# Kernel optimization log

Hardware: AMD Instinct MI355X
Metric: run time of the kernel (lower is better)

Reference implementation:

```python
import jax, jax.numpy as jnp
import numpy as np

N_PROP = 2048
N_CLS = 81  # background + 80 foreground classes
IMG_W, IMG_H = 1333.0, 800.0
SCORE_THRESH = 0.05
NMS_THRESH = 0.5
DET_PER_IMG = 100
BBOX_CLIP = float(np.log(1000.0 / 16.0))
TO_REMOVE = 1.0


def setup_inputs() -> dict:
    key = jax.random.key(0)
    k1, k2, k3, k4, k5, k6 = jax.random.split(key, 6)
    class_logits = jax.random.normal(k1, (N_PROP, N_CLS), jnp.float32)
    box_regression = jax.random.normal(k2, (N_PROP, N_CLS * 4), jnp.float32)
    # valid xyxy proposals inside the image
    x1 = jax.random.uniform(k3, (N_PROP,), jnp.float32, 0.0, IMG_W * 0.7)
    y1 = jax.random.uniform(k4, (N_PROP,), jnp.float32, 0.0, IMG_H * 0.7)
    w = jax.random.uniform(k5, (N_PROP,), jnp.float32, 16.0, IMG_W * 0.3)
    h = jax.random.uniform(k6, (N_PROP,), jnp.float32, 16.0, IMG_H * 0.3)
    proposals = jnp.stack([x1, y1, x1 + w, y1 + h], axis=-1)
    return {"class_logits": class_logits, "box_regression": box_regression, "proposals": proposals}


def decode_boxes(reg, props):
    # BoxCoder.decode with weights (10,10,5,5); reg: [N, C*4] -> [N, C, 4]
    widths = props[:, 2] - props[:, 0] + TO_REMOVE
    heights = props[:, 3] - props[:, 1] + TO_REMOVE
    ctr_x = props[:, 0] + 0.5 * widths
    ctr_y = props[:, 1] + 0.5 * heights
    r = reg.reshape(reg.shape[0], -1, 4)
    dx = r[..., 0] / 10.0
    dy = r[..., 1] / 10.0
    dw = jnp.minimum(r[..., 2] / 5.0, BBOX_CLIP)
    dh = jnp.minimum(r[..., 3] / 5.0, BBOX_CLIP)
    pcx = dx * widths[:, None] + ctr_x[:, None]
    pcy = dy * heights[:, None] + ctr_y[:, None]
    pw = jnp.exp(dw) * widths[:, None]
    ph = jnp.exp(dh) * heights[:, None]
    return jnp.stack([pcx - 0.5 * pw, pcy - 0.5 * ph,
                      pcx + 0.5 * pw - TO_REMOVE, pcy + 0.5 * ph - TO_REMOVE], axis=-1)


def pairwise_iou(b):
    # b: [N,4] xyxy -> [N,N] IoU with +1 pixel convention
    area = (b[:, 2] - b[:, 0] + TO_REMOVE) * (b[:, 3] - b[:, 1] + TO_REMOVE)
    lt = jnp.maximum(b[:, None, :2], b[None, :, :2])
    rb = jnp.minimum(b[:, None, 2:], b[None, :, 2:])
    wh = jnp.clip(rb - lt + TO_REMOVE, 0.0)
    inter = wh[..., 0] * wh[..., 1]
    return inter / (area[:, None] + area[None, :] - inter)


def nms_keep(boxes, scores, valid, thresh):
    # returns boolean keep mask (fixed shape) equivalent to greedy NMS on valid boxes
    n = scores.shape[0]
    order = jnp.argsort(-scores)
    b = boxes[order]
    v = valid[order]
    iou = pairwise_iou(b)  # [N,N]
    idx = jnp.arange(n)

    def step(suppressed, inp):
        row, vi, i = inp
        keep_i = vi & jnp.logical_not(suppressed[i])
        suppressed = suppressed | (keep_i & (row > thresh) & (idx > i))
        return suppressed, keep_i

    _, keep_sorted = jax.lax.scan(step, jnp.zeros(n, bool), (iou, v, idx))
    return jnp.zeros(n, bool).at[order].set(keep_sorted)


def _forward(class_logits, box_regression, proposals):
    probs = jax.nn.softmax(class_logits, axis=-1)          # [N, C]
    boxes = decode_boxes(box_regression, proposals)        # [N, C, 4]
    # clip_to_image (remove_empty=False)
    boxes = jnp.stack([jnp.clip(boxes[..., 0], 0.0, IMG_W - TO_REMOVE),
                       jnp.clip(boxes[..., 1], 0.0, IMG_H - TO_REMOVE),
                       jnp.clip(boxes[..., 2], 0.0, IMG_W - TO_REMOVE),
                       jnp.clip(boxes[..., 3], 0.0, IMG_H - TO_REMOVE)], axis=-1)
    # drop background class 0; class-major layout [C-1, N, ...]
    boxes_c = jnp.transpose(boxes[:, 1:, :], (1, 0, 2))    # [C-1, N, 4]
    scores_c = probs[:, 1:].T                              # [C-1, N]
    valid = scores_c > SCORE_THRESH
    keep = jax.vmap(nms_keep, in_axes=(0, 0, 0, None))(boxes_c, scores_c, valid, NMS_THRESH)
    masked = jnp.where(keep, scores_c, -1.0)               # invalid -> below any prob
    flat_scores = masked.reshape(-1)                       # [(C-1)*N]
    _, top_idx = jax.lax.top_k(flat_scores, DET_PER_IMG)
    out_scores = flat_scores[top_idx]
    out_boxes = boxes_c.reshape(-1, 4)[top_idx]
    out_labels = top_idx // N_PROP + 1                     # class labels in [1, C-1]
    return out_boxes, out_scores, out_labels


def reference(class_logits, box_regression, proposals):
    return _forward(class_logits, box_regression, proposals)
```

## Files before the change

kernel.cpp:

```cpp
#include <hip/hip_runtime.h>
#include <math.h>

#define NPROP 2048
#define NCLS 81
#define NFG 80
#define CAP 512
#define TOPC 100
#define NB 1152
#define BMIN 0x7A99


#define LDS_FENCE() do { __builtin_amdgcn_wave_barrier(); \
    asm volatile("s_waitcnt lgkmcnt(0)" ::: "memory");     \
    __builtin_amdgcn_wave_barrier(); } while (0)

__device__ __forceinline__ void decode_clip(const float* __restrict__ props,
                                            const float* __restrict__ reg,
                                            int p, int cls, float out[4]) {
    float px1 = props[p * 4 + 0], py1 = props[p * 4 + 1];
    float px2 = props[p * 4 + 2], py2 = props[p * 4 + 3];
    float w = px2 - px1 + 1.0f;
    float h = py2 - py1 + 1.0f;
    float cx = px1 + 0.5f * w;
    float cy = py1 + 0.5f * h;
    const float* r = reg + (size_t)p * (NCLS * 4) + cls * 4;
    float dx = r[0] / 10.0f;
    float dy = r[1] / 10.0f;
    float dw = fminf(r[2] / 5.0f, 4.135166556742356f);
    float dh = fminf(r[3] / 5.0f, 4.135166556742356f);
    float pcx = dx * w + cx;
    float pcy = dy * h + cy;
    float pw = expf(dw) * w;
    float ph = expf(dh) * h;
    float x1 = pcx - 0.5f * pw;
    float y1 = pcy - 0.5f * ph;
    float x2 = pcx + 0.5f * pw - 1.0f;
    float y2 = pcy + 0.5f * ph - 1.0f;
    out[0] = fminf(fmaxf(x1, 0.0f), 1332.0f);
    out[1] = fminf(fmaxf(y1, 0.0f), 799.0f);
    out[2] = fminf(fmaxf(x2, 0.0f), 1332.0f);
    out[3] = fminf(fmaxf(y2, 0.0f), 799.0f);
}

__global__ __launch_bounds__(256) void softmax_scatter(const float* __restrict__ logits,
                                                       unsigned long long* __restrict__ cand) {
    int gw = (blockIdx.x * blockDim.x + threadIdx.x) >> 6;
    int lane = threadIdx.x & 63;
    if (gw >= NPROP) return;
    const float* row = logits + (size_t)gw * NCLS;
    float a = row[lane];
    bool hasb = (lane + 64) < NCLS;
    float b = hasb ? row[lane + 64] : -INFINITY;
    float m = fmaxf(a, b);
    #pragma unroll
    for (int s = 32; s; s >>= 1) m = fmaxf(m, __shfl_xor(m, s));
    float ea = expf(a - m);
    float eb = hasb ? expf(b - m) : 0.0f;
    float sum = ea + eb;
    #pragma unroll
    for (int s = 32; s; s >>= 1) sum += __shfl_xor(sum, s);
    float pa = ea / sum;
    float pb = eb / sum;
    unsigned int np = (unsigned int)(~gw);
    if (lane != 0) {
        cand[(size_t)(lane - 1) * NPROP + gw] = (pa > 0.05f)
            ? (((unsigned long long)__float_as_uint(pa) << 32) | np) : 0ULL;
    }
    if (hasb) {
        cand[(size_t)(lane + 63) * NPROP + gw] = (pb > 0.05f)
            ? (((unsigned long long)__float_as_uint(pb) << 32) | np) : 0ULL;
    }
}

__global__ __launch_bounds__(64) void nms_kernel(const unsigned long long* __restrict__ cand,
                                                 const float* __restrict__ props,
                                                 const float* __restrict__ reg,
                                                 int* __restrict__ scnt,
                                                 unsigned long long* __restrict__ surv) {
    const int c = blockIdx.x;
    const int lane = threadIdx.x;
    __shared__ unsigned long long keys[CAP];
    __shared__ float4 bxs[CAP];

    const unsigned long long* col = cand + (size_t)c * NPROP;
    unsigned long long v[32];
    #pragma unroll
    for (int t = 0; t < 32; ++t) v[t] = col[t * 64 + lane];

    int base = 0;
    #pragma unroll
    for (int t = 0; t < 32; ++t) {
        bool keep = v[t] != 0ULL;
        unsigned long long mask = __ballot(keep);
        if (keep) {
            int pos = base + __popcll(mask & ((1ULL << lane) - 1ULL));
            if (pos < CAP) keys[pos] = v[t];
        }
        base += __popcll(mask);
    }
    int M = base > CAP ? CAP : base;
    int nsurv = 0;
    if (M > 0) {
        int S = 64;
        while (S < M) S <<= 1;
        for (int i = lane; i < S; i += 64)
            if (i >= M) keys[i] = 0ULL;
        LDS_FENCE();

        for (int k = 2; k <= S; k <<= 1) {
            for (int j = k >> 1; j > 0; j >>= 1) {
                for (int i = lane; i < S; i += 64) {
                    int l = i ^ j;
                    if (l > i) {
                        unsigned long long A = keys[i], B = keys[l];
                        bool dir = ((i & k) == 0);
                        if ((A < B) == dir) { keys[i] = B; keys[l] = A; }
                    }
                }
                LDS_FENCE();
            }
        }

        float4 myb[8];
        #pragma unroll
        for (int ns = 0; ns < 8; ++ns) {
            int idx = lane + ns * 64;
            if (idx < M) {
                unsigned long long key = keys[idx];
                int p = (int)(~(unsigned int)key);
                float b4[4];
                decode_clip(props, reg, p, c + 1, b4);
                float4 f = make_float4(b4[0], b4[1], b4[2], b4[3]);
                myb[ns] = f;
                bxs[idx] = f;
            }
        }
        LDS_FENCE();

        unsigned int my_sup = 0u;
        for (int i = 0; i < M; ++i) {
            int owner = i & 63, slot = i >> 6;
            unsigned int os = __shfl(my_sup, owner);
            if ((os >> slot) & 1u) continue;
            float4 bi = bxs[i];
            float ai = (bi.z - bi.x + 1.0f) * (bi.w - bi.y + 1.0f);
            #pragma unroll
            for (int ns = 0; ns < 8; ++ns) {
                int j = lane + ns * 64;
                if (j < M && j > i) {
                    float4 bj = myb[ns];
                    float aj = (bj.z - bj.x + 1.0f) * (bj.w - bj.y + 1.0f);
                    float ltx = fmaxf(bi.x, bj.x), lty = fmaxf(bi.y, bj.y);
                    float rbx = fminf(bi.z, bj.z), rby = fminf(bi.w, bj.w);
                    float iw = fmaxf(rbx - ltx + 1.0f, 0.0f);
                    float ih = fmaxf(rby - lty + 1.0f, 0.0f);
                    float inter = iw * ih;
                    float iou = inter / (ai + aj - inter);
                    if (iou > 0.5f) my_sup |= (1u << ns);
                }
            }
        }

        #pragma unroll
        for (int ns = 0; ns < 8; ++ns) {
            if (ns * 64 >= M) break;
            int j = lane + ns * 64;
            bool keep = (j < M) && !((my_sup >> ns) & 1u);
            unsigned long long mask = __ballot(keep);
            if (keep) {
                int pos = nsurv + __popcll(mask & ((1ULL << lane) - 1ULL));
                if (pos < TOPC) {
                    unsigned long long key = keys[j];
                    int p = (int)(~(unsigned int)key);
                    unsigned int flat = (unsigned int)(c * NPROP + p);
                    surv[c * TOPC + pos] =
                        (key & 0xFFFFFFFF00000000ULL) | (unsigned int)(~flat);
                }
            }
            nsurv += __popcll(mask);
        }
    }
    if (lane == 0) scnt[c] = nsurv;
}

__global__ __launch_bounds__(256) void topk_kernel(const int* __restrict__ scnt,
                                                   const unsigned long long* __restrict__ surv,
                                                   const float* __restrict__ props,
                                                   const float* __restrict__ reg,
                                                   float* __restrict__ out) {
    __shared__ unsigned int hist[NB];
    __shared__ unsigned long long comp[1024];
    __shared__ int s_n[NFG];
    __shared__ int sB;
    __shared__ int compN;
    const int tid = threadIdx.x;

    for (int i = tid; i < NB; i += 256) hist[i] = 0u;
    if (tid < NFG) {
        int k = scnt[tid];
        s_n[tid] = (k > TOPC) ? TOPC : k;
    }
    if (tid == 0) compN = 0;
    __syncthreads();

    for (int idx = tid; idx < NFG * TOPC; idx += 256) {
        int cc = idx / TOPC, i = idx - cc * TOPC;
        if (i < s_n[cc]) {
            unsigned long long key = surv[idx];
            int b = (int)(((unsigned int)(key >> 32)) >> 15) - BMIN;
            b = b < 0 ? 0 : (b >= NB ? NB - 1 : b);
            atomicAdd(&hist[b], 1u);
        }
    }
    __syncthreads();

    if (tid < 64) {
        int running = 0, Bstar = 0;
        bool found = false;
        for (int chunk = NB - 64; chunk >= 0; chunk -= 64) {
            int b = chunk + 63 - tid;
            int s = (int)hist[b];
            #pragma unroll
            for (int d = 1; d < 64; d <<= 1) {
                int o = __shfl_up(s, d);
                if (tid >= d) s += o;
            }
            int cum = running + s;
            unsigned long long m = __ballot(cum >= TOPC);
            if (m != 0ULL) {
                int l = (int)__ffsll((unsigned long long)m) - 1;
                Bstar = chunk + 63 - l;
                found = true;
                break;
            }
            running += __shfl(s, 63);
        }
        if (!found) Bstar = 0;
        if (tid == 0) sB = Bstar;
    }
    __syncthreads();
    int Bstar = sB;

    for (int idx = tid; idx < NFG * TOPC; idx += 256) {
        int cc = idx / TOPC, i = idx - cc * TOPC;
        if (i < s_n[cc]) {
            unsigned long long key = surv[idx];
            int b = (int)(((unsigned int)(key >> 32)) >> 15) - BMIN;
            b = b < 0 ? 0 : (b >= NB ? NB - 1 : b);
            if (b >= Bstar) {
                int pos = atomicAdd(&compN, 1);
                if (pos < 1024) comp[pos] = key;
            }
        }
    }
    __syncthreads();
    int K = compN;
    if (K > 1024) K = 1024;
    int P = 128;
    while (P < K) P <<= 1;
    for (int i = K + tid; i < P; i += 256) comp[i] = 0ULL;
    __syncthreads();

    if (tid < 64) {
        for (int k = 2; k <= P; k <<= 1) {
            for (int j = k >> 1; j > 0; j >>= 1) {
                for (int i = tid; i < P; i += 64) {
                    int l = i ^ j;
                    if (l > i) {
                        unsigned long long A = comp[i], B = comp[l];
                        bool dir = ((i & k) == 0);
                        if ((A < B) == dir) { comp[i] = B; comp[l] = A; }
                    }
                }
                LDS_FENCE();
            }
        }
    }
    __syncthreads();

    if (tid < TOPC) {
        unsigned long long key = comp[tid];
        float score;
        int flat;
        if (key == 0ULL) {
            score = -1.0f;
            flat = tid;
        } else {
            score = __uint_as_float((unsigned int)(key >> 32));
            flat = (int)(~(unsigned int)key);
        }
        int cc = flat >> 11;
        int p = flat & (NPROP - 1);
        float b4[4];
        decode_clip(props, reg, p, cc + 1, b4);
        out[tid * 4 + 0] = b4[0];
        out[tid * 4 + 1] = b4[1];
        out[tid * 4 + 2] = b4[2];
        out[tid * 4 + 3] = b4[3];
        out[400 + tid] = score;
        out[500 + tid] = (float)(cc + 1);
    }
}

extern "C" void kernel_launch(void* const* d_in, const int* in_sizes, int n_in,
                              void* d_out, int out_size, void* d_ws, size_t ws_size,
                              hipStream_t stream) {
    const float* logits = (const float*)d_in[0];
    const float* reg    = (const float*)d_in[1];
    const float* props  = (const float*)d_in[2];
    float* out = (float*)d_out;

    int* scnt = (int*)d_ws;
    unsigned long long* surv = (unsigned long long*)((char*)d_ws + 384);
    unsigned long long* cand = (unsigned long long*)((char*)d_ws + 65536);

    hipLaunchKernelGGL(softmax_scatter, dim3((NPROP * 64) / 256), dim3(256), 0, stream,
                       logits, cand);
    hipLaunchKernelGGL(nms_kernel, dim3(NFG), dim3(64), 0, stream,
                       cand, props, reg, scnt, surv);
    hipLaunchKernelGGL(topk_kernel, dim3(1), dim3(256), 0, stream,
                       scnt, surv, props, reg, out);
}
```

Before: 131.1 us.

## Stage softmax scatter through LDS and bulk-load NMS columns with 256 threads

The softmax kernel now handles 8 rows per block and stages its class-major candidate keys in shared memory. It then writes them out as runs of 8 consecutive 64-bit words per class instead of scattered single words per row. The NMS kernel uses 256 threads to copy its 2048-entry column into LDS with 128-bit loads before one wave compacts it. The aim is better coalescing of the transposed writes and faster column loads, at the cost of extra LDS traffic, a barrier, and idle waves after the copy.

```diff
diff --git a/kernel.cpp b/kernel.cpp
--- a/kernel.cpp
+++ b/kernel.cpp
@@ -8,6 +8,7 @@
 #define TOPC 100
 #define NB 1152
 #define BMIN 0x7A99
+#define RPB 8
 
 
 #define LDS_FENCE() do { __builtin_amdgcn_wave_barrier(); \
@@ -44,57 +45,76 @@
 
 __global__ __launch_bounds__(256) void softmax_scatter(const float* __restrict__ logits,
                                                        unsigned long long* __restrict__ cand) {
-    int gw = (blockIdx.x * blockDim.x + threadIdx.x) >> 6;
-    int lane = threadIdx.x & 63;
-    if (gw >= NPROP) return;
-    const float* row = logits + (size_t)gw * NCLS;
-    float a = row[lane];
-    bool hasb = (lane + 64) < NCLS;
-    float b = hasb ? row[lane + 64] : -INFINITY;
-    float m = fmaxf(a, b);
+    __shared__ unsigned long long skey[NFG][RPB + 1];
+    const int tid = threadIdx.x;
+    const int lane = tid & 63;
+    const int w = tid >> 6;
+    const int rbase = blockIdx.x * RPB;
+
     #pragma unroll
-    for (int s = 32; s; s >>= 1) m = fmaxf(m, __shfl_xor(m, s));
-    float ea = expf(a - m);
-    float eb = hasb ? expf(b - m) : 0.0f;
-    float sum = ea + eb;
-    #pragma unroll
-    for (int s = 32; s; s >>= 1) sum += __shfl_xor(sum, s);
-    float pa = ea / sum;
-    float pb = eb / sum;
-    unsigned int np = (unsigned int)(~gw);
-    if (lane != 0) {
-        cand[(size_t)(lane - 1) * NPROP + gw] = (pa > 0.05f)
-            ? (((unsigned long long)__float_as_uint(pa) << 32) | np) : 0ULL;
-    }
-    if (hasb) {
-        cand[(size_t)(lane + 63) * NPROP + gw] = (pb > 0.05f)
-            ? (((unsigned long long)__float_as_uint(pb) << 32) | np) : 0ULL;
-    }
-}
-
-__global__ __launch_bounds__(64) void nms_kernel(const unsigned long long* __restrict__ cand,
-                                                 const float* __restrict__ props,
-                                                 const float* __restrict__ reg,
-                                                 int* __restrict__ scnt,
-                                                 unsigned long long* __restrict__ surv) {
+    for (int rr = 0; rr < 2; ++rr) {
+        int rib = w * 2 + rr;
+        int row = rbase + rib;
+        const float* lrow = logits + (size_t)row * NCLS;
+        float a = lrow[lane];
+        bool hasb = (lane + 64) < NCLS;
+        float b = hasb ? lrow[lane + 64] : -INFINITY;
+        float m = fmaxf(a, b);
+        #pragma unroll
+        for (int s = 32; s; s >>= 1) m = fmaxf(m, __shfl_xor(m, s));
+        float ea = expf(a - m);
+        float eb = hasb ? expf(b - m) : 0.0f;
+        float sum = ea + eb;
+        #pragma unroll
+        for (int s = 32; s; s >>= 1) sum += __shfl_xor(sum, s);
+        float pa = ea / sum;
+        float pb = eb / sum;
+        unsigned int np = (unsigned int)(~row);
+        if (lane != 0) {
+            skey[lane - 1][rib] = (pa > 0.05f)
+                ? (((unsigned long long)__float_as_uint(pa) << 32) | np) : 0ULL;
+        }
+        if (hasb) {
+            skey[lane + 63][rib] = (pb > 0.05f)
+                ? (((unsigned long long)__float_as_uint(pb) << 32) | np) : 0ULL;
+        }
+    }
+    __syncthreads();
+
+    for (int idx = tid; idx < NFG * RPB; idx += 256) {
+        int c = idx >> 3, j = idx & 7;
+        cand[(size_t)c * NPROP + rbase + j] = skey[c][j];
+    }
+}
+
+__global__ __launch_bounds__(256) void nms_kernel(const unsigned long long* __restrict__ cand,
+                                                  const float* __restrict__ props,
+                                                  const float* __restrict__ reg,
+                                                  int* __restrict__ scnt,
+                                                  unsigned long long* __restrict__ surv) {
     const int c = blockIdx.x;
-    const int lane = threadIdx.x;
+    const int tid = threadIdx.x;
+    const int lane = tid & 63;
+    __shared__ unsigned long long colL[NPROP];
     __shared__ unsigned long long keys[CAP];
     __shared__ float4 bxs[CAP];
 
-    const unsigned long long* col = cand + (size_t)c * NPROP;
-    unsigned long long v[32];
+    const ulonglong2* col2 = (const ulonglong2*)(cand + (size_t)c * NPROP);
+    ulonglong2* lds2 = (ulonglong2*)colL;
     #pragma unroll
-    for (int t = 0; t < 32; ++t) v[t] = col[t * 64 + lane];
+    for (int t = 0; t < 4; ++t)
+        lds2[t * 256 + tid] = col2[t * 256 + tid];
+    __syncthreads();
+    if (tid >= 64) return;
 
     int base = 0;
-    #pragma unroll
     for (int t = 0; t < 32; ++t) {
-        bool keep = v[t] != 0ULL;
+        unsigned long long key = colL[t * 64 + lane];
+        bool keep = key != 0ULL;
         unsigned long long mask = __ballot(keep);
         if (keep) {
             int pos = base + __popcll(mask & ((1ULL << lane) - 1ULL));
-            if (pos < CAP) keys[pos] = v[t];
+            if (pos < CAP) keys[pos] = key;
         }
         base += __popcll(mask);
     }
@@ -314,9 +334,9 @@
     unsigned long long* surv = (unsigned long long*)((char*)d_ws + 384);
     unsigned long long* cand = (unsigned long long*)((char*)d_ws + 65536);
 
-    hipLaunchKernelGGL(softmax_scatter, dim3((NPROP * 64) / 256), dim3(256), 0, stream,
+    hipLaunchKernelGGL(softmax_scatter, dim3(NPROP / RPB), dim3(256), 0, stream,
                        logits, cand);
-    hipLaunchKernelGGL(nms_kernel, dim3(NFG), dim3(64), 0, stream,
+    hipLaunchKernelGGL(nms_kernel, dim3(NFG), dim3(256), 0, stream,
                        cand, props, reg, scnt, surv);
     hipLaunchKernelGGL(topk_kernel, dim3(1), dim3(256), 0, stream,
                        scnt, surv, props, reg, out);
```

New measurement: 132.3 us. Within noise of the previous version (+0.9%).
